# Optimization experiments

Measured on AMD Instinct MI355X. Metric: run time of the kernel, lower is better.

The kernel has to match this reference:

```python
import jax, jax.numpy as jnp
import numpy as np

N = 50000      # num_nodes
E = 800000     # num_edges (before self loops)
EMB = 128      # emb_dim
GH = 64        # gcn_hidden
TD = 4         # temporal_dim
B = 64         # batch of sequences
T = 200        # max sequence length
H = 128        # lstm_hidden (per direction)
IN_DIM = 2 + EMB + TD


def lstm_scan(x_tbi, w_ih, w_hh, b_ih, b_hh):
    """x_tbi: [T, B, I] -> hidden states [T, B, H]. PyTorch gate order i,f,g,o."""
    Bsz = x_tbi.shape[1]
    Hh = w_hh.shape[1]

    def step(carry, xt):
        h, c = carry
        g = xt @ w_ih.T + h @ w_hh.T + b_ih + b_hh
        i, f, gg, o = jnp.split(g, 4, axis=-1)
        c = jax.nn.sigmoid(f) * c + jax.nn.sigmoid(i) * jnp.tanh(gg)
        h = jax.nn.sigmoid(o) * jnp.tanh(c)
        return (h, c), h

    init = (jnp.zeros((Bsz, Hh), x_tbi.dtype), jnp.zeros((Bsz, Hh), x_tbi.dtype))
    _, hs = jax.lax.scan(step, init, x_tbi)
    return hs


def gcn_layer(x, W, b, src, dst, ew):
    """PyG GCNConv: linear -> symmetric-norm gather/scatter-add -> bias.
    (self loops already appended to src/dst/ew by caller)"""
    h = x @ W  # [N, out]
    deg = jax.ops.segment_sum(ew, dst, num_segments=N)
    dinv = jnp.where(deg > 0, jax.lax.rsqrt(deg), 0.0)
    norm = dinv[src] * ew * dinv[dst]            # [E+N]
    msg = h[src] * norm[:, None]                  # gather + scale
    return jax.ops.segment_sum(msg, dst, num_segments=N) + b


def setup_inputs() -> dict:
    key = jax.random.key(0)
    ks = jax.random.split(key, 16)
    s = 0.02
    return {
        'x_coords': jax.random.normal(ks[0], (N, 2), jnp.float32),
        'temporal_features': jax.random.uniform(ks[1], (N, TD), jnp.float32, -1.0, 1.0),
        'edge_index': jax.random.randint(ks[2], (2, E), 0, N),
        'edge_weight': jnp.ones((E,), jnp.float32),
        'seq': jax.random.randint(ks[3], (B, T), 0, N),
        'lengths': jax.random.randint(ks[4], (B,), 1, T + 1),
        'node_emb': jax.random.normal(ks[5], (N, EMB), jnp.float32) * s,
        'gcn1_w': jax.random.normal(ks[6], (IN_DIM, GH), jnp.float32) * s,
        'gcn1_b': jnp.zeros((GH,), jnp.float32),
        'gcn2_w': jax.random.normal(ks[7], (GH, EMB), jnp.float32) * s,
        'gcn2_b': jnp.zeros((EMB,), jnp.float32),
        'w_ih_f': jax.random.normal(ks[8], (4 * H, EMB), jnp.float32) * s,
        'w_hh_f': jax.random.normal(ks[9], (4 * H, H), jnp.float32) * s,
        'b_ih_f': jnp.zeros((4 * H,), jnp.float32),
        'b_hh_f': jnp.zeros((4 * H,), jnp.float32),
        'w_ih_b': jax.random.normal(ks[10], (4 * H, EMB), jnp.float32) * s,
        'w_hh_b': jax.random.normal(ks[11], (4 * H, H), jnp.float32) * s,
        'b_ih_b': jnp.zeros((4 * H,), jnp.float32),
        'b_hh_b': jnp.zeros((4 * H,), jnp.float32),
        'attn_w': jax.random.normal(ks[12], (2 * H,), jnp.float32) * s,
        'attn_b': jnp.zeros((), jnp.float32),
        'fc_w': jax.random.normal(ks[13], (2 * H, N), jnp.float32) * s,
        'fc_b': jnp.zeros((N,), jnp.float32),
    }


def reference(x_coords, temporal_features, edge_index, edge_weight, seq, lengths,
              node_emb, gcn1_w, gcn1_b, gcn2_w, gcn2_b,
              w_ih_f, w_hh_f, b_ih_f, b_hh_f,
              w_ih_b, w_hh_b, b_ih_b, b_hh_b,
              attn_w, attn_b, fc_w, fc_b):
    # --- GCN with self loops (PyG add_self_loops=True, fill_value=1) ---
    loop = jnp.arange(N)
    src = jnp.concatenate([edge_index[0], loop])
    dst = jnp.concatenate([edge_index[1], loop])
    ew = jnp.concatenate([edge_weight, jnp.ones((N,), edge_weight.dtype)])

    x = jnp.concatenate([x_coords, node_emb, temporal_features], axis=1)  # [N, 134]
    z = jax.nn.relu(gcn_layer(x, gcn1_w, gcn1_b, src, dst, ew))
    z = gcn_layer(z, gcn2_w, gcn2_b, src, dst, ew)  # dropout = identity (eval)

    # --- sequence embedding + BiLSTM ---
    seq_emb = z[seq]                                  # [B, T, EMB]
    h_f = lstm_scan(seq_emb.transpose(1, 0, 2), w_ih_f, w_hh_f, b_ih_f, b_hh_f)
    h_f = h_f.transpose(1, 0, 2)                      # [B, T, H]

    # backward direction: reverse each sequence within its valid length
    t = jnp.arange(T)
    valid = t[None, :] < lengths[:, None]             # [B, T]
    rev_idx = jnp.where(valid, lengths[:, None] - 1 - t[None, :], t[None, :])
    x_rev = jnp.take_along_axis(seq_emb, rev_idx[:, :, None], axis=1)
    h_b = lstm_scan(x_rev.transpose(1, 0, 2), w_ih_b, w_hh_b, b_ih_b, b_hh_b)
    h_b = jnp.take_along_axis(h_b.transpose(1, 0, 2), rev_idx[:, :, None], axis=1)

    lstm_out = jnp.concatenate([h_f, h_b], axis=-1)   # [B, T, 2H]

    # --- masked attention pooling ---
    scores = lstm_out @ attn_w + attn_b               # [B, T]
    scores = jnp.where(valid, scores, -jnp.inf)
    aw = jax.nn.softmax(scores, axis=1)
    context = jnp.einsum('bt,btd->bd', aw, lstm_out)  # [B, 2H]

    return context @ fc_w + fc_b                      # [B, N]
```

## Files before the change

kernel.cpp:

```cpp
#include <hip/hip_runtime.h>
#include <math.h>

#define NN 50000
#define NE 800000
#define EMB 128
#define GH 64
#define BB 64
#define TT 200
#define HH 128
#define G4 512
#define IND 134
#define PM 128
#define PO 128

__device__ __forceinline__ float sigf(float x) { return 1.0f / (1.0f + __expf(-x)); }
__device__ __forceinline__ float tanhf_(float x) { return 1.0f - 2.0f / (__expf(2.0f * x) + 1.0f); }

__global__ void hist_kernel(const int* __restrict__ ei, const float* __restrict__ ew,
                            int* __restrict__ cnt, float* __restrict__ degw) {
    int e = blockIdx.x * 256 + threadIdx.x;
    if (e >= NE) return;
    int d = ei[NE + e];
    atomicAdd(&cnt[d], 1);
    atomicAdd(&degw[d], ew[e]);
}

__global__ __launch_bounds__(1024) void scan1_kernel(const int* __restrict__ cnt,
                                                     const float* __restrict__ degw,
                                                     float* __restrict__ dinv,
                                                     int* __restrict__ rs, int* __restrict__ partials) {
    __shared__ int s[1024];
    int gid = blockIdx.x * 1024 + threadIdx.x;
    int v = (gid < NN) ? cnt[gid] : 0;
    if (gid < NN) dinv[gid] = rsqrtf(degw[gid] + 1.0f);
    s[threadIdx.x] = v;
    __syncthreads();
    for (int off = 1; off < 1024; off <<= 1) {
        int add = (threadIdx.x >= (unsigned)off) ? s[threadIdx.x - off] : 0;
        __syncthreads();
        s[threadIdx.x] += add;
        __syncthreads();
    }
    if (gid < NN) rs[gid] = s[threadIdx.x] - v;
    if (threadIdx.x == 1023) partials[blockIdx.x] = s[1023];
}

__global__ void misc_kernel(int* __restrict__ partials, int nblk,
                            const float* __restrict__ W1, float* __restrict__ w1t) {
    int blk = blockIdx.x;
    int tid = threadIdx.x;
    if (blk == 0) {
        __shared__ int s[64];
        int v = (tid < nblk) ? partials[tid] : 0;
        s[tid] = v;
        __syncthreads();
        for (int off = 1; off < 64; off <<= 1) {
            int add = (tid >= off) ? s[tid - off] : 0;
            __syncthreads();
            s[tid] += add;
            __syncthreads();
        }
        if (tid < nblk) partials[tid] = s[tid] - v;
    } else {
        int i = (blk - 1) * 256 + tid;
        if (i < 64 * 136) {
            int o = i / 136, j = i - o * 136;
            float v = 0.0f;
            if (j < 128) v = W1[(size_t)(j + 2) * GH + o];
            else if (j < 130) v = W1[(size_t)(j - 128) * GH + o];
            else if (j < 134) v = W1[(size_t)j * GH + o];
            w1t[i] = v;
        }
    }
}

__global__ __launch_bounds__(256) void wcomb_kernel(const float* __restrict__ w_ih_f,
                                                    const float* __restrict__ w_ih_b,
                                                    const float* __restrict__ W2,
                                                    const float* __restrict__ b2,
                                                    const float* __restrict__ b_ih_f,
                                                    const float* __restrict__ b_hh_f,
                                                    const float* __restrict__ b_ih_b,
                                                    const float* __restrict__ b_hh_b,
                                                    float* __restrict__ wcomb,
                                                    float* __restrict__ bcomb) {
    int bx = blockIdx.x, tid = threadIdx.x;
    int dir = bx >> 7, o0 = (bx & 127) * 4;
    const float* w_ih = dir ? w_ih_b : w_ih_f;
    __shared__ __align__(16) float w2s[GH][EMB];
    __shared__ __align__(16) float wihs[4][EMB];
    __shared__ __align__(16) float b2s[EMB];
    for (int i = tid; i < GH * EMB / 4; i += 256)
        ((float4*)w2s)[i] = ((const float4*)W2)[i];
    for (int i = tid; i < 4 * EMB / 4; i += 256) {
        int oo = i >> 5, e4 = i & 31;
        ((float4*)wihs)[i] = *(const float4*)&w_ih[(size_t)(o0 + oo) * EMB + e4 * 4];
    }
    if (tid < 32) ((float4*)b2s)[tid] = ((const float4*)b2)[tid];
    __syncthreads();
    int oo = tid >> 6, k = tid & 63;
    float acc = 0.0f;
#pragma unroll 8
    for (int e4 = 0; e4 < 32; ++e4) {
        float4 a = *(const float4*)&wihs[oo][e4 * 4];
        float4 w = *(const float4*)&w2s[k][e4 * 4];
        acc += a.x * w.x + a.y * w.y + a.z * w.z + a.w * w.w;
    }
    wcomb[((size_t)dir * G4 + o0 + oo) * GH + k] = acc;
    if (tid < 4) {
        int o = o0 + tid;
        float s = dir ? (b_ih_b[o] + b_hh_b[o]) : (b_ih_f[o] + b_hh_f[o]);
        for (int e = 0; e < EMB; ++e) s += wihs[tid][e] * b2s[e];
        bcomb[dir * G4 + o] = s;
    }
}

__global__ __launch_bounds__(1024) void scan3_kernel(const int* __restrict__ partials,
                                                     int* __restrict__ rs, int* __restrict__ cursor) {
    int gid = blockIdx.x * 1024 + threadIdx.x;
    if (gid < NN) {
        int v = rs[gid] + partials[gid >> 10];
        rs[gid] = v;
        cursor[gid] = v;
    }
    if (gid == 0) rs[NN] = NE;
}

__global__ void fill_kernel(const int* __restrict__ ei, const float* __restrict__ ew,
                            const float* __restrict__ dinv, int* __restrict__ cursor,
                            int2* __restrict__ ssrcw) {
    int e = blockIdx.x * 256 + threadIdx.x;
    if (e >= NE) return;
    int s = ei[e], d = ei[NE + e];
    int pos = atomicAdd(&cursor[d], 1);
    ssrcw[pos] = make_int2(s, __float_as_int(ew[e] * dinv[s] * dinv[d]));
}

__global__ __launch_bounds__(256) void gemm1_kernel(const float* __restrict__ coords,
                                                    const float* __restrict__ temporal,
                                                    const float* __restrict__ emb,
                                                    const float* __restrict__ w1t,
                                                    float* __restrict__ h1) {
    __shared__ __align__(16) float xs[128][136];
    __shared__ __align__(16) float wt[64][136];
    int tid = threadIdx.x;
    int m0 = blockIdx.x * 128;
    for (int i = tid; i < 64 * 34; i += 256) {
        int rr = i / 34, w = i - rr * 34;
        float4 v = *(const float4*)&w1t[(size_t)rr * 136 + w * 4];
        int ws = (w < 32) ? (w ^ ((rr >> 3) & 7)) : w;
        *(float4*)&wt[rr][ws * 4] = v;
    }
    for (int i = tid; i < 128 * 32; i += 256) {
        int r = i >> 5, c4 = i & 31;
        int m = m0 + r;
        float4 v = make_float4(0.f, 0.f, 0.f, 0.f);
        if (m < NN) v = *(const float4*)&emb[(size_t)m * EMB + c4 * 4];
        *(float4*)&xs[r][(c4 ^ ((r >> 2) & 7)) * 4] = v;
    }
    for (int i = tid; i < 128 * 8; i += 256) {
        int r = i >> 3, c = i & 7;
        int m = m0 + r;
        float v = 0.0f;
        if (m < NN) {
            if (c < 2) v = coords[2 * m + c];
            else if (c < 6) v = temporal[4 * m + (c - 2)];
        }
        xs[r][128 + c] = v;
    }
    __syncthreads();
    int mt = tid >> 3, ot = tid & 7;
    int xswz = mt & 7, wswz = ot & 7;
    float acc[4][8];
#pragma unroll
    for (int mi = 0; mi < 4; ++mi)
#pragma unroll
        for (int oi = 0; oi < 8; ++oi) acc[mi][oi] = 0.0f;
    for (int k4 = 0; k4 < 34; ++k4) {
        int xk = (k4 < 32) ? (k4 ^ xswz) : k4;
        int wk = (k4 < 32) ? (k4 ^ wswz) : k4;
        float4 xv[4], wv[8];
#pragma unroll
        for (int mi = 0; mi < 4; ++mi) xv[mi] = *(const float4*)&xs[mt * 4 + mi][xk * 4];
#pragma unroll
        for (int oi = 0; oi < 8; ++oi) wv[oi] = *(const float4*)&wt[ot * 8 + oi][wk * 4];
#pragma unroll
        for (int mi = 0; mi < 4; ++mi)
#pragma unroll
            for (int oi = 0; oi < 8; ++oi)
                acc[mi][oi] += xv[mi].x * wv[oi].x + xv[mi].y * wv[oi].y
                             + xv[mi].z * wv[oi].z + xv[mi].w * wv[oi].w;
    }
#pragma unroll
    for (int mi = 0; mi < 4; ++mi) {
        int m = m0 + mt * 4 + mi;
        if (m >= NN) continue;
        int ob = ot * 8;
        *(float4*)&h1[(size_t)m * GH + ob] = make_float4(acc[mi][0], acc[mi][1], acc[mi][2], acc[mi][3]);
        *(float4*)&h1[(size_t)m * GH + ob + 4] = make_float4(acc[mi][4], acc[mi][5], acc[mi][6], acc[mi][7]);
    }
}

__global__ __launch_bounds__(256) void agg_kernel(const float* __restrict__ hin,
                                                  const int* __restrict__ rs,
                                                  const int2* __restrict__ ssrcw,
                                                  const float* __restrict__ dinv,
                                                  const float* __restrict__ bias, int relu,
                                                  float* __restrict__ hout) {
    int lane = threadIdx.x & 63;
    int wid = threadIdx.x >> 6;
    int n = blockIdx.x * 4 + wid;
    if (n >= NN) return;
    float dv = dinv[n];
    float acc = hin[(size_t)n * GH + lane] * (dv * dv);
    int2 range = *(const int2*)&rs[n];
    int i = range.x, e1 = range.y;
    for (; i + 7 < e1; i += 8) {
        int4 p0 = *(const int4*)&ssrcw[i];
        int4 p1 = *(const int4*)&ssrcw[i + 2];
        int4 p2 = *(const int4*)&ssrcw[i + 4];
        int4 p3 = *(const int4*)&ssrcw[i + 6];
        float a0 = hin[(size_t)p0.x * GH + lane];
        float a1 = hin[(size_t)p0.z * GH + lane];
        float a2 = hin[(size_t)p1.x * GH + lane];
        float a3 = hin[(size_t)p1.z * GH + lane];
        float a4 = hin[(size_t)p2.x * GH + lane];
        float a5 = hin[(size_t)p2.z * GH + lane];
        float a6 = hin[(size_t)p3.x * GH + lane];
        float a7 = hin[(size_t)p3.z * GH + lane];
        acc += a0 * __int_as_float(p0.y) + a1 * __int_as_float(p0.w)
             + a2 * __int_as_float(p1.y) + a3 * __int_as_float(p1.w)
             + a4 * __int_as_float(p2.y) + a5 * __int_as_float(p2.w)
             + a6 * __int_as_float(p3.y) + a7 * __int_as_float(p3.w);
    }
    for (; i + 3 < e1; i += 4) {
        int4 p0 = *(const int4*)&ssrcw[i];
        int4 p1 = *(const int4*)&ssrcw[i + 2];
        float a0 = hin[(size_t)p0.x * GH + lane];
        float a1 = hin[(size_t)p0.z * GH + lane];
        float a2 = hin[(size_t)p1.x * GH + lane];
        float a3 = hin[(size_t)p1.z * GH + lane];
        acc += a0 * __int_as_float(p0.y) + a1 * __int_as_float(p0.w)
             + a2 * __int_as_float(p1.y) + a3 * __int_as_float(p1.w);
    }
    for (; i < e1; ++i) {
        int2 p = ssrcw[i];
        acc += hin[(size_t)p.x * GH + lane] * __int_as_float(p.y);
    }
    if (bias) acc += bias[lane];
    if (relu) acc = fmaxf(acc, 0.0f);
    hout[(size_t)n * GH + lane] = acc;
}

__global__ __launch_bounds__(256) void pregemm_kernel(const float* __restrict__ a2,
                                                      const int* __restrict__ seq,
                                                      const float* __restrict__ wcomb,
                                                      const float* __restrict__ bcomb,
                                                      const int* __restrict__ lengths,
                                                      float* __restrict__ xpf,
                                                      float* __restrict__ xpb) {
    int dir = blockIdx.z;
    int o0 = blockIdx.y * PO;
    int m0 = blockIdx.x * PM;
    const float* wc = wcomb + (size_t)dir * G4 * GH;
    __shared__ __align__(16) float xs[PM][GH];
    __shared__ __align__(16) float ws[PO][GH];
    __shared__ float bsh[PO];
    int tid = threadIdx.x;
#pragma unroll
    for (int i = 0; i < 8; ++i) {
        int idx = i * 256 + tid;
        int row = idx >> 4, c4 = idx & 15;
        float4 v = *(const float4*)&wc[(size_t)(o0 + row) * GH + c4 * 4];
        *(float4*)&ws[row][(c4 ^ ((row >> 3) & 7)) * 4] = v;
    }
    if (tid < PO) bsh[tid] = bcomb[dir * G4 + o0 + tid];
#pragma unroll
    for (int i = 0; i < 8; ++i) {
        int idx = i * 256 + tid;
        int r = idx >> 4, c4 = idx & 15;
        int m = m0 + r;
        int t = m >> 6, b = m & 63;
        int tsrc = t;
        if (dir) { int len = lengths[b]; tsrc = (t < len) ? (len - 1 - t) : t; }
        int node = seq[b * TT + tsrc];
        float4 v = *(const float4*)&a2[(size_t)node * GH + c4 * 4];
        *(float4*)&xs[r][(c4 ^ ((r >> 3) & 3)) * 4] = v;
    }
    __syncthreads();
    int mt = tid >> 4, ot = tid & 15;
    int mswz = mt & 3, oswz = ot & 7;
    float acc[8][8];
#pragma unroll
    for (int mi = 0; mi < 8; ++mi)
#pragma unroll
        for (int oi = 0; oi < 8; ++oi) acc[mi][oi] = 0.0f;
    for (int k4 = 0; k4 < 16; ++k4) {
        int xk = (k4 ^ mswz) * 4;
        int wk = (k4 ^ oswz) * 4;
        float4 xv[8], wv[8];
#pragma unroll
        for (int mi = 0; mi < 8; ++mi) xv[mi] = *(const float4*)&xs[mt * 8 + mi][xk];
#pragma unroll
        for (int oi = 0; oi < 8; ++oi) wv[oi] = *(const float4*)&ws[ot * 8 + oi][wk];
#pragma unroll
        for (int mi = 0; mi < 8; ++mi)
#pragma unroll
            for (int oi = 0; oi < 8; ++oi)
                acc[mi][oi] += xv[mi].x * wv[oi].x + xv[mi].y * wv[oi].y
                             + xv[mi].z * wv[oi].z + xv[mi].w * wv[oi].w;
    }
    float* xp = dir ? xpb : xpf;
#pragma unroll
    for (int mi = 0; mi < 8; ++mi) {
        int m = m0 + mt * 8 + mi;
        int ob = ot * 8;
        float4 oa = make_float4(acc[mi][0] + bsh[ob + 0], acc[mi][1] + bsh[ob + 1],
                                acc[mi][2] + bsh[ob + 2], acc[mi][3] + bsh[ob + 3]);
        float4 obv = make_float4(acc[mi][4] + bsh[ob + 4], acc[mi][5] + bsh[ob + 5],
                                 acc[mi][6] + bsh[ob + 6], acc[mi][7] + bsh[ob + 7]);
        *(float4*)&xp[(size_t)m * G4 + o0 + ob] = oa;
        *(float4*)&xp[(size_t)m * G4 + o0 + ob + 4] = obv;
    }
}

#define PIN4(v) asm volatile("" : "+v"(v.x), "+v"(v.y), "+v"(v.z), "+v"(v.w))
__global__ __launch_bounds__(1024, 4) void lstm_kernel(const float* __restrict__ xpf,
                                                       const float* __restrict__ xpb,
                                                       const float* __restrict__ w_hh_f,
                                                       const float* __restrict__ w_hh_b,
                                                       const int* __restrict__ lengths,
                                                       float* __restrict__ hfo,
                                                       float* __restrict__ hbo) {
    int chain = blockIdx.x;
    int dir = chain & 1, b = chain >> 1;
    const float* w_hh = dir ? w_hh_b : w_hh_f;
    const float* xp = dir ? xpb : xpf;
    float* ho = dir ? hbo : hfo;
    int tid = threadIdx.x;
    int u = tid & 127;
    int kq = tid >> 7;
    int len = lengths[b];

    float4 W[4][4];
#pragma unroll
    for (int g = 0; g < 4; ++g)
#pragma unroll
        for (int j4 = 0; j4 < 4; ++j4) {
            W[g][j4] = *(const float4*)&w_hh[(size_t)(g * HH + u) * HH + kq * 16 + j4 * 4];
            PIN4(W[g][j4]);
        }

    __shared__ __align__(16) float hl[HH];
    __shared__ __align__(16) float part[8][HH][4];
    if (tid < HH) hl[tid] = 0.0f;
    __syncthreads();

    float cst = 0.0f, hkeep = 0.0f;
    int tprev = -1;
    float x0 = 0.f, x1 = 0.f, x2 = 0.f, x3 = 0.f;
    const float* xpt = xp + (size_t)b * G4 + u;
    if (tid < HH && len > 0) {
        x0 = xpt[0]; x1 = xpt[HH]; x2 = xpt[2 * HH]; x3 = xpt[3 * HH];
    }
    for (int t = 0; t < len; ++t) {
        float n0 = 0.f, n1 = 0.f, n2 = 0.f, n3 = 0.f;
        if (tid < HH) {
            if (tprev >= 0) ho[((size_t)b * TT + tprev) * HH + u] = hkeep;
            if (t + 1 < len) {
                const float* xn = xpt + (size_t)(t + 1) * (BB * G4);
                n0 = xn[0]; n1 = xn[HH]; n2 = xn[2 * HH]; n3 = xn[3 * HH];
            }
        }
        const float4* h4 = (const float4*)&hl[kq * 16];
        float a0 = 0.f, a1 = 0.f, a2 = 0.f, a3 = 0.f;
#pragma unroll
        for (int j4 = 0; j4 < 4; ++j4) {
            float4 hv = h4[j4];
            a0 += W[0][j4].x * hv.x + W[0][j4].y * hv.y + W[0][j4].z * hv.z + W[0][j4].w * hv.w;
            a1 += W[1][j4].x * hv.x + W[1][j4].y * hv.y + W[1][j4].z * hv.z + W[1][j4].w * hv.w;
            a2 += W[2][j4].x * hv.x + W[2][j4].y * hv.y + W[2][j4].z * hv.z + W[2][j4].w * hv.w;
            a3 += W[3][j4].x * hv.x + W[3][j4].y * hv.y + W[3][j4].z * hv.z + W[3][j4].w * hv.w;
        }
        if (kq) *(float4*)&part[kq][u][0] = make_float4(a0, a1, a2, a3);
        __syncthreads();
        if (tid < HH) {
            float s0 = x0 + a0, s1 = x1 + a1, s2 = x2 + a2, s3 = x3 + a3;
#pragma unroll
            for (int q = 1; q < 8; ++q) {
                float4 p = *(const float4*)&part[q][u][0];
                s0 += p.x; s1 += p.y; s2 += p.z; s3 += p.w;
            }
            float gi = sigf(s0), gf = sigf(s1), gg = tanhf_(s2), go = sigf(s3);
            cst = gf * cst + gi * gg;
            float h = go * tanhf_(cst);
            hl[u] = h;
            hkeep = h;
            tprev = dir ? (len - 1 - t) : t;
            x0 = n0; x1 = n1; x2 = n2; x3 = n3;
        }
        __syncthreads();
    }
    if (tid < HH && tprev >= 0) ho[((size_t)b * TT + tprev) * HH + u] = hkeep;
}

__global__ __launch_bounds__(256) void attn_kernel(const float* __restrict__ hf,
                                                   const float* __restrict__ hb,
                                                   const float* __restrict__ attn_w,
                                                   const float* __restrict__ attn_b,
                                                   const int* __restrict__ lengths,
                                                   float* __restrict__ ctx) {
    int b = blockIdx.x;
    int tid = threadIdx.x;
    int len = lengths[b];
    __shared__ __align__(16) float wl[256];
    __shared__ float pl[256];
    __shared__ float red[256];
    wl[tid] = attn_w[tid];
    __syncthreads();
    float sc = -3.0e38f;
    if (tid < len) {
        const float4* rf = (const float4*)(hf + ((size_t)b * TT + tid) * HH);
        const float4* rb = (const float4*)(hb + ((size_t)b * TT + tid) * HH);
        const float4* w4 = (const float4*)wl;
        float s = attn_b[0];
        for (int k4 = 0; k4 < 32; ++k4) {
            float4 a = rf[k4], ww = w4[k4];
            s += a.x * ww.x + a.y * ww.y + a.z * ww.z + a.w * ww.w;
        }
        for (int k4 = 0; k4 < 32; ++k4) {
            float4 a = rb[k4], ww = w4[32 + k4];
            s += a.x * ww.x + a.y * ww.y + a.z * ww.z + a.w * ww.w;
        }
        sc = s;
    }
    red[tid] = sc;
    __syncthreads();
    for (int off = 128; off > 0; off >>= 1) {
        if (tid < off) red[tid] = fmaxf(red[tid], red[tid + off]);
        __syncthreads();
    }
    float mx = red[0];
    __syncthreads();
    float e = (tid < len) ? __expf(sc - mx) : 0.0f;
    red[tid] = e;
    __syncthreads();
    for (int off = 128; off > 0; off >>= 1) {
        if (tid < off) red[tid] += red[tid + off];
        __syncthreads();
    }
    float inv = 1.0f / red[0];
    pl[tid] = e * inv;
    __syncthreads();
    float acc = 0.0f;
    const float* basep = (tid < HH) ? (hf + (size_t)b * TT * HH + tid)
                                    : (hb + (size_t)b * TT * HH + (tid - HH));
#pragma unroll 4
    for (int t = 0; t < len; ++t) acc += pl[t] * basep[(size_t)t * HH];
    ctx[(size_t)b * 256 + tid] = acc;
}

__global__ __launch_bounds__(256) void fc_kernel(const float* __restrict__ ctx,
                                                 const float* __restrict__ fc_w,
                                                 const float* __restrict__ fc_b,
                                                 float* __restrict__ out) {
    __shared__ __align__(16) float cl[64][256];
    for (int i = threadIdx.x; i < 64 * 256 / 4; i += 256)
        ((float4*)cl)[i] = ((const float4*)ctx)[i];
    __syncthreads();
    int lane = threadIdx.x & 63;
    int bq = threadIdx.x >> 6;
    int nb = blockIdx.x * 256 + lane;
    float acc[16][4];
#pragma unroll
    for (int i = 0; i < 16; ++i)
#pragma unroll
        for (int c = 0; c < 4; ++c) acc[i][c] = 0.0f;
    for (int k4 = 0; k4 < 64; ++k4) {
        int k = k4 * 4;
        float w[4][4];
#pragma unroll
        for (int j = 0; j < 4; ++j)
#pragma unroll
            for (int c = 0; c < 4; ++c) {
                int n = nb + c * 64;
                w[j][c] = (n < NN) ? fc_w[(size_t)(k + j) * NN + n] : 0.0f;
            }
#pragma unroll
        for (int i = 0; i < 16; ++i) {
            float4 cv = *(const float4*)&cl[bq * 16 + i][k];
#pragma unroll
            for (int c = 0; c < 4; ++c)
                acc[i][c] += cv.x * w[0][c] + cv.y * w[1][c] + cv.z * w[2][c] + cv.w * w[3][c];
        }
    }
#pragma unroll
    for (int i = 0; i < 16; ++i)
#pragma unroll
        for (int c = 0; c < 4; ++c) {
            int n = nb + c * 64;
            if (n < NN) out[(size_t)(bq * 16 + i) * NN + n] = acc[i][c] + fc_b[n];
        }
}

extern "C" void kernel_launch(void* const* d_in, const int* in_sizes, int n_in,
                              void* d_out, int out_size, void* d_ws, size_t ws_size,
                              hipStream_t stream) {
    const float* x_coords   = (const float*)d_in[0];
    const float* temporal   = (const float*)d_in[1];
    const int*   edge_index = (const int*)d_in[2];
    const float* edge_w     = (const float*)d_in[3];
    const int*   seq        = (const int*)d_in[4];
    const int*   lengths    = (const int*)d_in[5];
    const float* node_emb   = (const float*)d_in[6];
    const float* gcn1_w     = (const float*)d_in[7];
    const float* gcn1_b     = (const float*)d_in[8];
    const float* gcn2_w     = (const float*)d_in[9];
    const float* gcn2_b     = (const float*)d_in[10];
    const float* w_ih_f     = (const float*)d_in[11];
    const float* w_hh_f     = (const float*)d_in[12];
    const float* b_ih_f     = (const float*)d_in[13];
    const float* b_hh_f     = (const float*)d_in[14];
    const float* w_ih_b     = (const float*)d_in[15];
    const float* w_hh_b     = (const float*)d_in[16];
    const float* b_ih_b     = (const float*)d_in[17];
    const float* b_hh_b     = (const float*)d_in[18];
    const float* attn_w     = (const float*)d_in[19];
    const float* attn_b     = (const float*)d_in[20];
    const float* fc_w       = (const float*)d_in[21];
    const float* fc_b       = (const float*)d_in[22];
    float* out = (float*)d_out;

    char* base = (char*)d_ws;
    size_t off = 0;
    auto alloc = [&](size_t nbytes) -> void* {
        void* p = base + off;
        off = (off + nbytes + 255) & ~(size_t)255;
        return p;
    };
    int*   cnt     = (int*)alloc((size_t)2 * NN * 4);
    float* degw    = (float*)(cnt + NN);
    float* dinv    = (float*)alloc((size_t)NN * 4);
    int*   rs      = (int*)alloc(((size_t)NN + 1) * 4);
    int*   cursor  = (int*)alloc((size_t)NN * 4);
    int*   partials= (int*)alloc(64 * 4);
    int2*  ssrcw   = (int2*)alloc((size_t)NE * 8);
    float* h1      = (float*)alloc((size_t)NN * GH * 4);
    float* z1      = (float*)alloc((size_t)NN * GH * 4);
    float* a2      = h1;
    float* w1t     = (float*)alloc((size_t)64 * 136 * 4);
    float* wcomb   = (float*)alloc((size_t)2 * G4 * GH * 4);
    float* bcomb   = (float*)alloc((size_t)2 * G4 * 4);
    float* xpf     = (float*)alloc((size_t)TT * BB * G4 * 4);
    float* xpb     = (float*)alloc((size_t)TT * BB * G4 * 4);
    float* hfo     = (float*)alloc((size_t)BB * TT * HH * 4);
    float* hbo     = (float*)alloc((size_t)BB * TT * HH * 4);
    float* ctx     = (float*)alloc((size_t)BB * 256 * 4);
    (void)ws_size; (void)in_sizes; (void)n_in; (void)out_size;

    hipMemsetAsync(cnt, 0, (size_t)2 * NN * 4, stream);

    hist_kernel<<<(NE + 255) / 256, 256, 0, stream>>>(edge_index, edge_w, cnt, degw);
    const int nblk = (NN + 1023) / 1024;
    scan1_kernel<<<nblk, 1024, 0, stream>>>(cnt, degw, dinv, rs, partials);
    misc_kernel<<<35, 256, 0, stream>>>(partials, nblk, gcn1_w, w1t);
    wcomb_kernel<<<256, 256, 0, stream>>>(w_ih_f, w_ih_b, gcn2_w, gcn2_b,
                                          b_ih_f, b_hh_f, b_ih_b, b_hh_b, wcomb, bcomb);
    scan3_kernel<<<nblk, 1024, 0, stream>>>(partials, rs, cursor);
    fill_kernel<<<(NE + 255) / 256, 256, 0, stream>>>(edge_index, edge_w, dinv, cursor, ssrcw);

    gemm1_kernel<<<(NN + 127) / 128, 256, 0, stream>>>(x_coords, temporal, node_emb, w1t, h1);
    agg_kernel<<<(NN + 3) / 4, 256, 0, stream>>>(h1, rs, ssrcw, dinv, gcn1_b, 1, z1);
    agg_kernel<<<(NN + 3) / 4, 256, 0, stream>>>(z1, rs, ssrcw, dinv, (const float*)nullptr, 0, a2);

    pregemm_kernel<<<dim3(TT * BB / PM, G4 / PO, 2), 256, 0, stream>>>(
        a2, seq, wcomb, bcomb, lengths, xpf, xpb);
    lstm_kernel<<<BB * 2, 1024, 0, stream>>>(xpf, xpb, w_hh_f, w_hh_b, lengths, hfo, hbo);
    attn_kernel<<<BB, 256, 0, stream>>>(hfo, hbo, attn_w, attn_b, lengths, ctx);
    fc_kernel<<<(NN + 255) / 256, 256, 0, stream>>>(ctx, fc_w, fc_b, out);
}
```

Before: 568.7 us.

## Spread LSTM gate reduction across all waves and drop second per-step barrier

Each wave now finishes the gate reduction, activation and cell update for the 16 hidden units that match its own k-slice of h. The next step's h input therefore stays wave-local in LDS and needs no block-wide barrier. Partial sums are double-buffered by step parity and stored in a padded transposed layout, so one __syncthreads per timestep is enough. The serial 128-thread tail, where 8 partials were summed and gates evaluated per unit, is removed. The cost is redundant cell-state computation in paired waves, plus a reliance on wave-synchronous LDS ordering enforced through inline s_waitcnt.

```diff
diff --git a/kernel.cpp b/kernel.cpp
--- a/kernel.cpp
+++ b/kernel.cpp
@@ -338,41 +338,37 @@
     const float* xp = dir ? xpb : xpf;
     float* ho = dir ? hbo : hfo;
     int tid = threadIdx.x;
+    int w = tid >> 6, lane = tid & 63;
     int u = tid & 127;
     int kq = tid >> 7;
+    int uu = lane >> 2, g = lane & 3;
+    int x = (w >> 1) * 16 + uu;
     int len = lengths[b];
 
     float4 W[4][4];
 #pragma unroll
-    for (int g = 0; g < 4; ++g)
+    for (int gg = 0; gg < 4; ++gg)
 #pragma unroll
         for (int j4 = 0; j4 < 4; ++j4) {
-            W[g][j4] = *(const float4*)&w_hh[(size_t)(g * HH + u) * HH + kq * 16 + j4 * 4];
-            PIN4(W[g][j4]);
-        }
-
-    __shared__ __align__(16) float hl[HH];
-    __shared__ __align__(16) float part[8][HH][4];
-    if (tid < HH) hl[tid] = 0.0f;
+            W[gg][j4] = *(const float4*)&w_hh[(size_t)(gg * HH + u) * HH + kq * 16 + j4 * 4];
+            PIN4(W[gg][j4]);
+        }
+
+    __shared__ __align__(16) float part[2][128][33];
+    __shared__ __align__(16) float hlw[16][16];
+    __shared__ __align__(16) float actw[16][16][4];
+    if (lane < 16) hlw[w][lane] = 0.0f;
     __syncthreads();
 
     float cst = 0.0f, hkeep = 0.0f;
     int tprev = -1;
-    float x0 = 0.f, x1 = 0.f, x2 = 0.f, x3 = 0.f;
-    const float* xpt = xp + (size_t)b * G4 + u;
-    if (tid < HH && len > 0) {
-        x0 = xpt[0]; x1 = xpt[HH]; x2 = xpt[2 * HH]; x3 = xpt[3 * HH];
-    }
+    bool hwriter = ((w & 1) == 0) && (g == 0);
+    const float* xbase = xp + (size_t)b * G4 + g * HH + x;
+    float xcur = xbase[0];
     for (int t = 0; t < len; ++t) {
-        float n0 = 0.f, n1 = 0.f, n2 = 0.f, n3 = 0.f;
-        if (tid < HH) {
-            if (tprev >= 0) ho[((size_t)b * TT + tprev) * HH + u] = hkeep;
-            if (t + 1 < len) {
-                const float* xn = xpt + (size_t)(t + 1) * (BB * G4);
-                n0 = xn[0]; n1 = xn[HH]; n2 = xn[2 * HH]; n3 = xn[3 * HH];
-            }
-        }
-        const float4* h4 = (const float4*)&hl[kq * 16];
+        if (hwriter && tprev >= 0) ho[((size_t)b * TT + tprev) * HH + x] = hkeep;
+        float xnext = (t + 1 < len) ? xbase[(size_t)(t + 1) * (BB * G4)] : 0.0f;
+        const float4* h4 = (const float4*)&hlw[w][0];
         float a0 = 0.f, a1 = 0.f, a2 = 0.f, a3 = 0.f;
 #pragma unroll
         for (int j4 = 0; j4 < 4; ++j4) {
@@ -382,26 +378,28 @@
             a2 += W[2][j4].x * hv.x + W[2][j4].y * hv.y + W[2][j4].z * hv.z + W[2][j4].w * hv.w;
             a3 += W[3][j4].x * hv.x + W[3][j4].y * hv.y + W[3][j4].z * hv.z + W[3][j4].w * hv.w;
         }
-        if (kq) *(float4*)&part[kq][u][0] = make_float4(a0, a1, a2, a3);
+        float* pw = &part[t & 1][u][kq];
+        pw[0]  = a0;
+        pw[8]  = a1;
+        pw[16] = a2;
+        pw[24] = a3;
         __syncthreads();
-        if (tid < HH) {
-            float s0 = x0 + a0, s1 = x1 + a1, s2 = x2 + a2, s3 = x3 + a3;
-#pragma unroll
-            for (int q = 1; q < 8; ++q) {
-                float4 p = *(const float4*)&part[q][u][0];
-                s0 += p.x; s1 += p.y; s2 += p.z; s3 += p.w;
-            }
-            float gi = sigf(s0), gf = sigf(s1), gg = tanhf_(s2), go = sigf(s3);
-            cst = gf * cst + gi * gg;
-            float h = go * tanhf_(cst);
-            hl[u] = h;
-            hkeep = h;
-            tprev = dir ? (len - 1 - t) : t;
-            x0 = n0; x1 = n1; x2 = n2; x3 = n3;
-        }
-        __syncthreads();
-    }
-    if (tid < HH && tprev >= 0) ho[((size_t)b * TT + tprev) * HH + u] = hkeep;
+        const float4* pr = (const float4*)&part[t & 1][x][g * 8];
+        float4 q0 = pr[0], q1 = pr[1];
+        float s = ((q0.x + q0.y) + (q0.z + q0.w)) + ((q1.x + q1.y) + (q1.z + q1.w)) + xcur;
+        float act = (g == 2) ? tanhf_(s) : sigf(s);
+        actw[w][uu][g] = act;
+        asm volatile("s_waitcnt lgkmcnt(0)" ::: "memory");
+        float4 av = *(const float4*)&actw[w][uu][0];
+        cst = av.y * cst + av.x * av.z;
+        float h = av.w * tanhf_(cst);
+        if (g == 0) hlw[w][uu] = h;
+        asm volatile("s_waitcnt lgkmcnt(0)" ::: "memory");
+        hkeep = h;
+        tprev = dir ? (len - 1 - t) : t;
+        xcur = xnext;
+    }
+    if (hwriter && tprev >= 0) ho[((size_t)b * TT + tprev) * HH + x] = hkeep;
 }
 
 __global__ __launch_bounds__(256) void attn_kernel(const float* __restrict__ hf,
```

New measurement: 747.2 us. 31.4% more time.
